# Kernel optimization log

Measured on AMD Instinct MI355X. Metric: run time of the kernel, lower is better.

Reference implementation:

```python
import jax, jax.numpy as jnp
import numpy as np

B, C, F, T, D = 8, 128, 256, 128, 32


def setup_inputs() -> dict:
    key = jax.random.key(0)
    ks = jax.random.split(key, 7)
    x = jax.random.normal(ks[0], (B, C, F, T), jnp.float32)
    # 1x1 Conv2d over the T axis == linear map on T; weights [out, T], bias [out]
    Wk = jax.random.normal(ks[1], (D, T), jnp.float32) * 0.05
    bk = jax.random.normal(ks[2], (D,), jnp.float32) * 0.05
    Wq = jax.random.normal(ks[3], (D, T), jnp.float32) * 0.05
    bq = jax.random.normal(ks[4], (D,), jnp.float32) * 0.05
    Wv = jax.random.normal(ks[5], (T, T), jnp.float32) * 0.05
    bv = jax.random.normal(ks[6], (T,), jnp.float32) * 0.05
    return {"x": x, "Wk": Wk, "bk": bk, "Wq": Wq, "bq": bq, "Wv": Wv, "bv": bv}


def _proj(xp, W, b):
    # xp: [B, C2, F, T]; W: [out, T] -> [B, F, out, C2]
    return jnp.einsum('bcft,dt->bfdc', xp, W) + b[None, None, :, None]


def reference(x, Wk, bk, Wq, bq, Wv, bv):
    C2 = x.shape[1] // 2
    xr, xi = x[:, :C2], x[:, C2:]
    k_r = _proj(xr, Wk, bk)  # [B,F,D,C2]
    k_i = _proj(xi, Wk, bk)
    q_r = _proj(xr, Wq, bq)
    q_i = _proj(xi, Wq, bq)
    v_r = _proj(xr, Wv, bv)  # [B,F,T,C2]
    v_i = _proj(xi, Wv, bv)
    # complex P = k^H... actually plain k^T q (no conjugate in source)
    P_r = jnp.einsum('bfdc,bfde->bfce', k_r, q_r) - jnp.einsum('bfdc,bfde->bfce', k_i, q_i)
    P_i = jnp.einsum('bfdc,bfde->bfce', k_r, q_i) + jnp.einsum('bfdc,bfde->bfce', k_i, q_r)
    # independent softmaxes over dim=2 (the first C2 axis)
    W_r = jax.nn.softmax(P_r, axis=2)
    W_i = jax.nn.softmax(P_i, axis=2)
    # output = v @ W (complex)
    o_r = jnp.einsum('bftc,bfce->bfte', v_r, W_r) - jnp.einsum('bftc,bfce->bfte', v_i, W_i)
    o_i = jnp.einsum('bftc,bfce->bfte', v_r, W_i) + jnp.einsum('bftc,bfce->bfte', v_i, W_r)
    # permute [B,F,T,C2] -> [B,C2,F,T], concat real/imag on channel axis
    o_r = jnp.transpose(o_r, (0, 3, 1, 2))
    o_i = jnp.transpose(o_i, (0, 3, 1, 2))
    return jnp.concatenate([o_r, o_i], axis=1)  # [B,C,F,T]
```

## Files before the change

### kernel.cpp

```cpp
#include <hip/hip_runtime.h>

typedef __attribute__((ext_vector_type(8))) __bf16 bf16x8;
typedef __attribute__((ext_vector_type(8))) unsigned short ushort8;
typedef __attribute__((ext_vector_type(4))) unsigned short ushort4v;
typedef __attribute__((ext_vector_type(4))) float f32x4;

namespace {
constexpr int kB = 8, kC = 128, kF = 256, kT = 128;

__device__ __forceinline__ int addrXT(int t, int p) { return t * 128 + (p ^ ((t & 7) << 3)); }
__device__ __forceinline__ int addrU(int ri, int e, int s) { return ri * 8192 + e * 128 + (s ^ ((e & 7) << 3)); }
__device__ __forceinline__ int addrK(int m, int c, int p) { return 16384 + m * 2048 + c * 32 + (p ^ ((c & 3) << 3)); }

__device__ __forceinline__ unsigned short b16(float f) {
    __bf16 h = (__bf16)f;
    return __builtin_bit_cast(unsigned short, h);
}

__device__ __forceinline__ bf16x8 ldfrag(const unsigned short* lds, int idx) {
    return __builtin_bit_cast(bf16x8, *(const ushort8*)(lds + idx));
}

__device__ __forceinline__ bf16x8 fneg(bf16x8 a) {
    ushort8 u = __builtin_bit_cast(ushort8, a);
    u ^= (unsigned short)0x8000;
    return __builtin_bit_cast(bf16x8, u);
}

__device__ __forceinline__ bf16x8 fragWg(const float* p) {
    f32x4 a = *(const f32x4*)p;
    f32x4 c = *(const f32x4*)(p + 4);
    bf16x8 r;
    r[0] = (__bf16)a[0]; r[1] = (__bf16)a[1]; r[2] = (__bf16)a[2]; r[3] = (__bf16)a[3];
    r[4] = (__bf16)c[0]; r[5] = (__bf16)c[1]; r[6] = (__bf16)c[2]; r[7] = (__bf16)c[3];
    return r;
}
}

__global__ __launch_bounds__(256, 4)
void chanattn_mfma2(const float* __restrict__ x,
                    const float* __restrict__ Wk, const float* __restrict__ bk,
                    const float* __restrict__ Wq, const float* __restrict__ bq,
                    const float* __restrict__ Wv, const float* __restrict__ bv,
                    float* __restrict__ out)
{
    __shared__ __align__(16) unsigned short lds[20480];

    const int f = blockIdx.x, b = blockIdx.y;
    const int tid = threadIdx.x;
    const int lane = tid & 63;
    const int w = tid >> 6;
    const int lr = lane & 15;
    const int lg = lane >> 4;
    const size_t cstr = (size_t)kF * kT;
    const float* xb = x + ((size_t)b * kC * kF + f) * kT;

    bf16x8 bqr, bqi;
    {
        bf16x8 xr_f[4], xi_f[4];
        #pragma unroll
        for (int ks = 0; ks < 4; ++ks) {
            xr_f[ks] = fragWg(xb + (size_t)(16 * w + lr) * cstr + ks * 32 + 8 * lg);
            xi_f[ks] = fragWg(xb + (size_t)(64 + 16 * w + lr) * cstr + ks * 32 + 8 * lg);
        }
        f32x4 qacc[2][2], kacc[2][2];
        #pragma unroll
        for (int ri = 0; ri < 2; ++ri)
            #pragma unroll
            for (int dt = 0; dt < 2; ++dt) {
                qacc[ri][dt] = (f32x4){0.f, 0.f, 0.f, 0.f};
                kacc[ri][dt] = (f32x4){0.f, 0.f, 0.f, 0.f};
            }
        #pragma unroll
        for (int dt = 0; dt < 2; ++dt)
            #pragma unroll
            for (int ks = 0; ks < 4; ++ks) {
                bf16x8 wq = fragWg(Wq + (size_t)(16 * dt + lr) * kT + ks * 32 + 8 * lg);
                bf16x8 wk = fragWg(Wk + (size_t)(16 * dt + lr) * kT + ks * 32 + 8 * lg);
                qacc[0][dt] = __builtin_amdgcn_mfma_f32_16x16x32_bf16(wq, xr_f[ks], qacc[0][dt], 0, 0, 0);
                qacc[1][dt] = __builtin_amdgcn_mfma_f32_16x16x32_bf16(wq, xi_f[ks], qacc[1][dt], 0, 0, 0);
                kacc[0][dt] = __builtin_amdgcn_mfma_f32_16x16x32_bf16(xr_f[ks], wk, kacc[0][dt], 0, 0, 0);
                kacc[1][dt] = __builtin_amdgcn_mfma_f32_16x16x32_bf16(xi_f[ks], wk, kacc[1][dt], 0, 0, 0);
            }
        const float bk0 = bk[lr], bk1 = bk[16 + lr];
        #pragma unroll
        for (int dt = 0; dt < 2; ++dt) {
            const int pcol = 8 * ((lr >> 2) & 3) + 4 * dt + (lr & 3);
            const float bb = dt ? bk1 : bk0;
            #pragma unroll
            for (int r = 0; r < 4; ++r) {
                const int c = 16 * w + 4 * lg + r;
                lds[addrK(0, c, pcol)] = b16(kacc[0][dt][r] + bb);
                lds[addrK(1, c, pcol)] = b16(kacc[1][dt][r] + bb);
            }
        }
        #pragma unroll
        for (int j = 0; j < 8; ++j) {
            const int dt = j >> 2, r = j & 3;
            const float bb = bq[16 * dt + 4 * lg + r];
            bqr[j] = (__bf16)(qacc[0][dt][r] + bb);
            bqi[j] = (__bf16)(qacc[1][dt][r] + bb);
        }
    }

    {
        const int c0 = 4 * (tid & 31);
        const int t0 = 4 * (tid >> 5);
        const int h  = c0 >> 6;
        const int cc = c0 & 63;
        const int p0 = 64 * h + 32 * (cc >> 5) + 8 * ((cc >> 2) & 3) + 4 * ((cc >> 4) & 1);
        #pragma unroll
        for (int tp = 0; tp < 4; ++tp) {
            const int t = t0 + 32 * tp;
            f32x4 v[4];
            #pragma unroll
            for (int j = 0; j < 4; ++j)
                v[j] = *(const f32x4*)(xb + (size_t)(c0 + j) * cstr + t);
            #pragma unroll
            for (int i = 0; i < 4; ++i) {
                ushort4v pk;
                pk[0] = b16(v[0][i]); pk[1] = b16(v[1][i]);
                pk[2] = b16(v[2][i]); pk[3] = b16(v[3][i]);
                *(ushort4v*)&lds[addrXT(t + i, p0)] = pk;
            }
        }
    }
    __syncthreads();

    f32x4 pr[4], pi[4];
    float inv_r, inv_i;
    {
        const f32x4 zero = {0.f, 0.f, 0.f, 0.f};
        #pragma unroll
        for (int ct = 0; ct < 4; ++ct) {
            bf16x8 akr = ldfrag(lds, addrK(0, ct * 16 + lr, 8 * lg));
            bf16x8 aki = ldfrag(lds, addrK(1, ct * 16 + lr, 8 * lg));
            pr[ct] = __builtin_amdgcn_mfma_f32_16x16x32_bf16(akr, bqr, zero, 0, 0, 0);
            pr[ct] = __builtin_amdgcn_mfma_f32_16x16x32_bf16(fneg(aki), bqi, pr[ct], 0, 0, 0);
            pi[ct] = __builtin_amdgcn_mfma_f32_16x16x32_bf16(akr, bqi, zero, 0, 0, 0);
            pi[ct] = __builtin_amdgcn_mfma_f32_16x16x32_bf16(aki, bqr, pi[ct], 0, 0, 0);
        }
        float mr = -1e30f, mi = -1e30f;
        #pragma unroll
        for (int ct = 0; ct < 4; ++ct)
            #pragma unroll
            for (int r = 0; r < 4; ++r) { mr = fmaxf(mr, pr[ct][r]); mi = fmaxf(mi, pi[ct][r]); }
        mr = fmaxf(mr, __shfl_xor(mr, 16)); mr = fmaxf(mr, __shfl_xor(mr, 32));
        mi = fmaxf(mi, __shfl_xor(mi, 16)); mi = fmaxf(mi, __shfl_xor(mi, 32));
        float sr = 0.f, si = 0.f;
        #pragma unroll
        for (int ct = 0; ct < 4; ++ct)
            #pragma unroll
            for (int r = 0; r < 4; ++r) {
                float er = __expf(pr[ct][r] - mr); pr[ct][r] = er; sr += er;
                float ei = __expf(pi[ct][r] - mi); pi[ct][r] = ei; si += ei;
            }
        sr += __shfl_xor(sr, 16); sr += __shfl_xor(sr, 32);
        si += __shfl_xor(si, 16); si += __shfl_xor(si, 32);
        inv_r = 1.f / sr; inv_i = 1.f / si;
    }

    bf16x8 awr[2], awi[2], awin[2];
    #pragma unroll
    for (int ks = 0; ks < 2; ++ks) {
        #pragma unroll
        for (int j = 0; j < 8; ++j) {
            const int ct = 2 * ks + (j >> 2), r = j & 3;
            awr[ks][j] = (__bf16)(pr[ct][r] * inv_r);
            awi[ks][j] = (__bf16)(pi[ct][r] * inv_i);
        }
        awin[ks] = fneg(awi[ks]);
    }

    f32x4 uacc_r[8], uacc_i[8];
    #pragma unroll
    for (int nt = 0; nt < 8; ++nt) {
        f32x4 ur = {0.f, 0.f, 0.f, 0.f}, ui = {0.f, 0.f, 0.f, 0.f};
        #pragma unroll
        for (int ks = 0; ks < 2; ++ks) {
            bf16x8 bxr = ldfrag(lds, addrXT(nt * 16 + lr, ks * 32 + 8 * lg));
            bf16x8 bxi = ldfrag(lds, addrXT(nt * 16 + lr, 64 + ks * 32 + 8 * lg));
            ur = __builtin_amdgcn_mfma_f32_16x16x32_bf16(awr[ks], bxr, ur, 0, 0, 0);
            ur = __builtin_amdgcn_mfma_f32_16x16x32_bf16(awin[ks], bxi, ur, 0, 0, 0);
            ui = __builtin_amdgcn_mfma_f32_16x16x32_bf16(awi[ks], bxr, ui, 0, 0, 0);
            ui = __builtin_amdgcn_mfma_f32_16x16x32_bf16(awr[ks], bxi, ui, 0, 0, 0);
        }
        uacc_r[nt] = ur; uacc_i[nt] = ui;
    }
    __syncthreads();
    #pragma unroll
    for (int nt = 0; nt < 8; ++nt)
        #pragma unroll
        for (int r = 0; r < 4; ++r) {
            const int e = 16 * w + 4 * lg + r;
            lds[addrU(0, e, nt * 16 + lr)] = b16(uacc_r[nt][r]);
            lds[addrU(1, e, nt * 16 + lr)] = b16(uacc_i[nt][r]);
        }
    __syncthreads();

    {
        #pragma unroll
        for (int mi_ = 0; mi_ < 2; ++mi_) {
            const int mt = 2 * w + mi_;
            bf16x8 av[4];
            #pragma unroll
            for (int ks = 0; ks < 4; ++ks)
                av[ks] = fragWg(Wv + (size_t)(mt * 16 + lr) * kT + ks * 32 + 8 * lg);
            float bvv[4];
            #pragma unroll
            for (int r = 0; r < 4; ++r) bvv[r] = 2.f * bv[mt * 16 + 4 * lg + r];

            #pragma unroll
            for (int et = 0; et < 4; ++et) {
                f32x4 aor = {0.f, 0.f, 0.f, 0.f}, aoi = {0.f, 0.f, 0.f, 0.f};
                #pragma unroll
                for (int ks = 0; ks < 4; ++ks) {
                    bf16x8 bur = ldfrag(lds, addrU(0, et * 16 + lr, ks * 32 + 8 * lg));
                    bf16x8 bui = ldfrag(lds, addrU(1, et * 16 + lr, ks * 32 + 8 * lg));
                    aor = __builtin_amdgcn_mfma_f32_16x16x32_bf16(av[ks], bur, aor, 0, 0, 0);
                    aoi = __builtin_amdgcn_mfma_f32_16x16x32_bf16(av[ks], bui, aoi, 0, 0, 0);
                }
                const int e = et * 16 + lr;
                const int tp0 = mt * 16 + 4 * lg;
                f32x4 vi;
                #pragma unroll
                for (int r = 0; r < 4; ++r) vi[r] = aoi[r] + bvv[r];
                *(f32x4*)(out + (((size_t)b * kC + e) * kF + f) * kT + tp0)      = aor;
                *(f32x4*)(out + (((size_t)b * kC + 64 + e) * kF + f) * kT + tp0) = vi;
            }
        }
    }
}

extern "C" void kernel_launch(void* const* d_in, const int* in_sizes, int n_in,
                              void* d_out, int out_size, void* d_ws, size_t ws_size,
                              hipStream_t stream) {
    const float* x  = (const float*)d_in[0];
    const float* Wk = (const float*)d_in[1];
    const float* bk = (const float*)d_in[2];
    const float* Wq = (const float*)d_in[3];
    const float* bq = (const float*)d_in[4];
    const float* Wv = (const float*)d_in[5];
    const float* bv = (const float*)d_in[6];
    float* out = (float*)d_out;

    dim3 grid(kF, kB);
    dim3 block(256);
    chanattn_mfma2<<<grid, block, 0, stream>>>(x, Wk, bk, Wq, bq, Wv, bv, out);
}
```

Measured before the change: 97.59 us.

## Pre-convert weights to bf16 fragment layout and hoist global loads earlier

Adds a small prologue kernel that converts Wk, Wq and Wv to bf16 in MFMA fragment order in the workspace, so the main kernel loads contiguous 16-byte fragments instead of converting fp32 weights per block. The x tile loads used for the LDS transpose are issued at kernel start, and the Wv fragments and bias are loaded before the barrier, so their latency overlaps with compute. The cost is an extra kernel launch and more live registers, which could reduce occupancy under the 4-blocks launch bound.

```diff
diff --git a/kernel.cpp b/kernel.cpp
--- a/kernel.cpp
+++ b/kernel.cpp
@@ -17,8 +17,8 @@
     return __builtin_bit_cast(unsigned short, h);
 }
 
-__device__ __forceinline__ bf16x8 ldfrag(const unsigned short* lds, int idx) {
-    return __builtin_bit_cast(bf16x8, *(const ushort8*)(lds + idx));
+__device__ __forceinline__ bf16x8 ldfrag(const unsigned short* p, int idx) {
+    return __builtin_bit_cast(bf16x8, *(const ushort8*)(p + idx));
 }
 
 __device__ __forceinline__ bf16x8 fneg(bf16x8 a) {
@@ -37,11 +37,30 @@
 }
 }
 
+__global__ __launch_bounds__(256)
+void conv_weights(const float* __restrict__ Wk, const float* __restrict__ Wq,
+                  const float* __restrict__ Wv, unsigned short* __restrict__ ws)
+{
+    const int fid = blockIdx.x * 256 + threadIdx.x;
+    if (fid >= 3072) return;
+    const float* src;
+    int local;
+    if (fid < 512)       { src = Wk; local = fid; }
+    else if (fid < 1024) { src = Wq; local = fid - 512; }
+    else                 { src = Wv; local = fid - 1024; }
+    const int lr = local & 15, lg = (local >> 4) & 3, ks = (local >> 6) & 3, tile = local >> 8;
+    const float* p = src + (size_t)(16 * tile + lr) * kT + ks * 32 + 8 * lg;
+    ushort8 o;
+    #pragma unroll
+    for (int j = 0; j < 8; ++j) o[j] = b16(p[j]);
+    *(ushort8*)(ws + (size_t)fid * 8) = o;
+}
+
 __global__ __launch_bounds__(256, 4)
-void chanattn_mfma2(const float* __restrict__ x,
-                    const float* __restrict__ Wk, const float* __restrict__ bk,
-                    const float* __restrict__ Wq, const float* __restrict__ bq,
-                    const float* __restrict__ Wv, const float* __restrict__ bv,
+void chanattn_mfma3(const float* __restrict__ x,
+                    const float* __restrict__ bk, const float* __restrict__ bq,
+                    const float* __restrict__ bv,
+                    const unsigned short* __restrict__ wsu,
                     float* __restrict__ out)
 {
     __shared__ __align__(16) unsigned short lds[20480];
@@ -55,14 +74,17 @@
     const size_t cstr = (size_t)kF * kT;
     const float* xb = x + ((size_t)b * kC * kF + f) * kT;
 
+    const int c0 = 4 * (tid & 31);
+    const int t0 = 4 * (tid >> 5);
+    f32x4 xv[4][4];
+    #pragma unroll
+    for (int tp = 0; tp < 4; ++tp)
+        #pragma unroll
+        for (int j = 0; j < 4; ++j)
+            xv[tp][j] = *(const f32x4*)(xb + (size_t)(c0 + j) * cstr + t0 + 32 * tp);
+
     bf16x8 bqr, bqi;
     {
-        bf16x8 xr_f[4], xi_f[4];
-        #pragma unroll
-        for (int ks = 0; ks < 4; ++ks) {
-            xr_f[ks] = fragWg(xb + (size_t)(16 * w + lr) * cstr + ks * 32 + 8 * lg);
-            xi_f[ks] = fragWg(xb + (size_t)(64 + 16 * w + lr) * cstr + ks * 32 + 8 * lg);
-        }
         f32x4 qacc[2][2], kacc[2][2];
         #pragma unroll
         for (int ri = 0; ri < 2; ++ri)
@@ -72,16 +94,19 @@
                 kacc[ri][dt] = (f32x4){0.f, 0.f, 0.f, 0.f};
             }
         #pragma unroll
-        for (int dt = 0; dt < 2; ++dt)
-            #pragma unroll
-            for (int ks = 0; ks < 4; ++ks) {
-                bf16x8 wq = fragWg(Wq + (size_t)(16 * dt + lr) * kT + ks * 32 + 8 * lg);
-                bf16x8 wk = fragWg(Wk + (size_t)(16 * dt + lr) * kT + ks * 32 + 8 * lg);
-                qacc[0][dt] = __builtin_amdgcn_mfma_f32_16x16x32_bf16(wq, xr_f[ks], qacc[0][dt], 0, 0, 0);
-                qacc[1][dt] = __builtin_amdgcn_mfma_f32_16x16x32_bf16(wq, xi_f[ks], qacc[1][dt], 0, 0, 0);
-                kacc[0][dt] = __builtin_amdgcn_mfma_f32_16x16x32_bf16(xr_f[ks], wk, kacc[0][dt], 0, 0, 0);
-                kacc[1][dt] = __builtin_amdgcn_mfma_f32_16x16x32_bf16(xi_f[ks], wk, kacc[1][dt], 0, 0, 0);
-            }
+        for (int ks = 0; ks < 4; ++ks) {
+            bf16x8 xr_f = fragWg(xb + (size_t)(16 * w + lr) * cstr + ks * 32 + 8 * lg);
+            bf16x8 xi_f = fragWg(xb + (size_t)(64 + 16 * w + lr) * cstr + ks * 32 + 8 * lg);
+            #pragma unroll
+            for (int dt = 0; dt < 2; ++dt) {
+                bf16x8 wk = ldfrag(wsu, (((dt * 4 + ks) * 4 + lg) * 16 + lr) * 8);
+                bf16x8 wq = ldfrag(wsu, 4096 + (((dt * 4 + ks) * 4 + lg) * 16 + lr) * 8);
+                qacc[0][dt] = __builtin_amdgcn_mfma_f32_16x16x32_bf16(wq, xr_f, qacc[0][dt], 0, 0, 0);
+                qacc[1][dt] = __builtin_amdgcn_mfma_f32_16x16x32_bf16(wq, xi_f, qacc[1][dt], 0, 0, 0);
+                kacc[0][dt] = __builtin_amdgcn_mfma_f32_16x16x32_bf16(xr_f, wk, kacc[0][dt], 0, 0, 0);
+                kacc[1][dt] = __builtin_amdgcn_mfma_f32_16x16x32_bf16(xi_f, wk, kacc[1][dt], 0, 0, 0);
+            }
+        }
         const float bk0 = bk[lr], bk1 = bk[16 + lr];
         #pragma unroll
         for (int dt = 0; dt < 2; ++dt) {
@@ -104,23 +129,17 @@
     }
 
     {
-        const int c0 = 4 * (tid & 31);
-        const int t0 = 4 * (tid >> 5);
         const int h  = c0 >> 6;
         const int cc = c0 & 63;
         const int p0 = 64 * h + 32 * (cc >> 5) + 8 * ((cc >> 2) & 3) + 4 * ((cc >> 4) & 1);
         #pragma unroll
         for (int tp = 0; tp < 4; ++tp) {
             const int t = t0 + 32 * tp;
-            f32x4 v[4];
-            #pragma unroll
-            for (int j = 0; j < 4; ++j)
-                v[j] = *(const f32x4*)(xb + (size_t)(c0 + j) * cstr + t);
             #pragma unroll
             for (int i = 0; i < 4; ++i) {
                 ushort4v pk;
-                pk[0] = b16(v[0][i]); pk[1] = b16(v[1][i]);
-                pk[2] = b16(v[2][i]); pk[3] = b16(v[3][i]);
+                pk[0] = b16(xv[tp][0][i]); pk[1] = b16(xv[tp][1][i]);
+                pk[2] = b16(xv[tp][2][i]); pk[3] = b16(xv[tp][3][i]);
                 *(ushort4v*)&lds[addrXT(t + i, p0)] = pk;
             }
         }
@@ -187,6 +206,19 @@
         }
         uacc_r[nt] = ur; uacc_i[nt] = ui;
     }
+
+    bf16x8 av[2][4];
+    float bvv[2][4];
+    #pragma unroll
+    for (int mi_ = 0; mi_ < 2; ++mi_) {
+        const int mt = 2 * w + mi_;
+        #pragma unroll
+        for (int ks = 0; ks < 4; ++ks)
+            av[mi_][ks] = ldfrag(wsu, 8192 + (((mt * 4 + ks) * 4 + lg) * 16 + lr) * 8);
+        #pragma unroll
+        for (int r = 0; r < 4; ++r) bvv[mi_][r] = 2.f * bv[mt * 16 + 4 * lg + r];
+    }
+
     __syncthreads();
     #pragma unroll
     for (int nt = 0; nt < 8; ++nt)
@@ -202,14 +234,6 @@
         #pragma unroll
         for (int mi_ = 0; mi_ < 2; ++mi_) {
             const int mt = 2 * w + mi_;
-            bf16x8 av[4];
-            #pragma unroll
-            for (int ks = 0; ks < 4; ++ks)
-                av[ks] = fragWg(Wv + (size_t)(mt * 16 + lr) * kT + ks * 32 + 8 * lg);
-            float bvv[4];
-            #pragma unroll
-            for (int r = 0; r < 4; ++r) bvv[r] = 2.f * bv[mt * 16 + 4 * lg + r];
-
             #pragma unroll
             for (int et = 0; et < 4; ++et) {
                 f32x4 aor = {0.f, 0.f, 0.f, 0.f}, aoi = {0.f, 0.f, 0.f, 0.f};
@@ -217,14 +241,14 @@
                 for (int ks = 0; ks < 4; ++ks) {
                     bf16x8 bur = ldfrag(lds, addrU(0, et * 16 + lr, ks * 32 + 8 * lg));
                     bf16x8 bui = ldfrag(lds, addrU(1, et * 16 + lr, ks * 32 + 8 * lg));
-                    aor = __builtin_amdgcn_mfma_f32_16x16x32_bf16(av[ks], bur, aor, 0, 0, 0);
-                    aoi = __builtin_amdgcn_mfma_f32_16x16x32_bf16(av[ks], bui, aoi, 0, 0, 0);
+                    aor = __builtin_amdgcn_mfma_f32_16x16x32_bf16(av[mi_][ks], bur, aor, 0, 0, 0);
+                    aoi = __builtin_amdgcn_mfma_f32_16x16x32_bf16(av[mi_][ks], bui, aoi, 0, 0, 0);
                 }
                 const int e = et * 16 + lr;
                 const int tp0 = mt * 16 + 4 * lg;
                 f32x4 vi;
                 #pragma unroll
-                for (int r = 0; r < 4; ++r) vi[r] = aoi[r] + bvv[r];
+                for (int r = 0; r < 4; ++r) vi[r] = aoi[r] + bvv[mi_][r];
                 *(f32x4*)(out + (((size_t)b * kC + e) * kF + f) * kT + tp0)      = aor;
                 *(f32x4*)(out + (((size_t)b * kC + 64 + e) * kF + f) * kT + tp0) = vi;
             }
@@ -243,8 +267,11 @@
     const float* Wv = (const float*)d_in[5];
     const float* bv = (const float*)d_in[6];
     float* out = (float*)d_out;
+    unsigned short* wsu = (unsigned short*)d_ws;
+
+    conv_weights<<<dim3(12), dim3(256), 0, stream>>>(Wk, Wq, Wv, wsu);
 
     dim3 grid(kF, kB);
     dim3 block(256);
-    chanattn_mfma2<<<grid, block, 0, stream>>>(x, Wk, bk, Wq, bq, Wv, bv, out);
-}
+    chanattn_mfma3<<<grid, block, 0, stream>>>(x, bk, bq, bv, wsu, out);
+}
```

After: 158.6 us. +62.5%, slower.

## Make V-projection stage wave-local and hoist x tile loads earlier

Applied to the files above, without the earlier changes.

The x tile staging loads are moved before the Q/K projection and all sixteen vector loads are issued up front, so more global loads are in flight. The U@W product now swaps the MFMA operands so each wave holds a transposed U tile. Each wave writes that tile into its own private LDS region, which removes the block-wide barrier before the final Wv projection; only a local lgkmcnt wait remains. Each wave then loops over all 8 T-tiles with its own 16 output channels. The trade-off is more Wv global loads per wave and more registers held for the early x loads.

```diff
diff --git a/kernel.cpp b/kernel.cpp
--- a/kernel.cpp
+++ b/kernel.cpp
@@ -9,16 +9,18 @@
 constexpr int kB = 8, kC = 128, kF = 256, kT = 128;
 
 __device__ __forceinline__ int addrXT(int t, int p) { return t * 128 + (p ^ ((t & 7) << 3)); }
-__device__ __forceinline__ int addrU(int ri, int e, int s) { return ri * 8192 + e * 128 + (s ^ ((e & 7) << 3)); }
 __device__ __forceinline__ int addrK(int m, int c, int p) { return 16384 + m * 2048 + c * 32 + (p ^ ((c & 3) << 3)); }
+__device__ __forceinline__ int addrUw(int w, int ri, int ep, int s) {
+    return w * 4096 + ri * 2048 + ep * 128 + (s ^ ((ep & 7) << 3));
+}
 
 __device__ __forceinline__ unsigned short b16(float f) {
     __bf16 h = (__bf16)f;
     return __builtin_bit_cast(unsigned short, h);
 }
 
-__device__ __forceinline__ bf16x8 ldfrag(const unsigned short* lds, int idx) {
-    return __builtin_bit_cast(bf16x8, *(const ushort8*)(lds + idx));
+__device__ __forceinline__ bf16x8 ldfrag(const unsigned short* p, int idx) {
+    return __builtin_bit_cast(bf16x8, *(const ushort8*)(p + idx));
 }
 
 __device__ __forceinline__ bf16x8 fneg(bf16x8 a) {
@@ -38,7 +40,7 @@
 }
 
 __global__ __launch_bounds__(256, 4)
-void chanattn_mfma2(const float* __restrict__ x,
+void chanattn_mfma4(const float* __restrict__ x,
                     const float* __restrict__ Wk, const float* __restrict__ bk,
                     const float* __restrict__ Wq, const float* __restrict__ bq,
                     const float* __restrict__ Wv, const float* __restrict__ bv,
@@ -55,6 +57,31 @@
     const size_t cstr = (size_t)kF * kT;
     const float* xb = x + ((size_t)b * kC * kF + f) * kT;
 
+    {
+        const int c0 = 4 * (tid & 31);
+        const int t0 = 4 * (tid >> 5);
+        const int h  = c0 >> 6;
+        const int cc = c0 & 63;
+        const int p0 = 64 * h + 32 * (cc >> 5) + 8 * ((cc >> 2) & 3) + 4 * ((cc >> 4) & 1);
+        f32x4 xv[4][4];
+        #pragma unroll
+        for (int tp = 0; tp < 4; ++tp)
+            #pragma unroll
+            for (int j = 0; j < 4; ++j)
+                xv[tp][j] = *(const f32x4*)(xb + (size_t)(c0 + j) * cstr + t0 + 32 * tp);
+        #pragma unroll
+        for (int tp = 0; tp < 4; ++tp) {
+            const int t = t0 + 32 * tp;
+            #pragma unroll
+            for (int i = 0; i < 4; ++i) {
+                ushort4v pk;
+                pk[0] = b16(xv[tp][0][i]); pk[1] = b16(xv[tp][1][i]);
+                pk[2] = b16(xv[tp][2][i]); pk[3] = b16(xv[tp][3][i]);
+                *(ushort4v*)&lds[addrXT(t + i, p0)] = pk;
+            }
+        }
+    }
+
     bf16x8 bqr, bqi;
     {
         bf16x8 xr_f[4], xi_f[4];
@@ -102,29 +129,6 @@
             bqi[j] = (__bf16)(qacc[1][dt][r] + bb);
         }
     }
-
-    {
-        const int c0 = 4 * (tid & 31);
-        const int t0 = 4 * (tid >> 5);
-        const int h  = c0 >> 6;
-        const int cc = c0 & 63;
-        const int p0 = 64 * h + 32 * (cc >> 5) + 8 * ((cc >> 2) & 3) + 4 * ((cc >> 4) & 1);
-        #pragma unroll
-        for (int tp = 0; tp < 4; ++tp) {
-            const int t = t0 + 32 * tp;
-            f32x4 v[4];
-            #pragma unroll
-            for (int j = 0; j < 4; ++j)
-                v[j] = *(const f32x4*)(xb + (size_t)(c0 + j) * cstr + t);
-            #pragma unroll
-            for (int i = 0; i < 4; ++i) {
-                ushort4v pk;
-                pk[0] = b16(v[0][i]); pk[1] = b16(v[1][i]);
-                pk[2] = b16(v[2][i]); pk[3] = b16(v[3][i]);
-                *(ushort4v*)&lds[addrXT(t + i, p0)] = pk;
-            }
-        }
-    }
     __syncthreads();
 
     f32x4 pr[4], pi[4];
@@ -180,55 +184,47 @@
         for (int ks = 0; ks < 2; ++ks) {
             bf16x8 bxr = ldfrag(lds, addrXT(nt * 16 + lr, ks * 32 + 8 * lg));
             bf16x8 bxi = ldfrag(lds, addrXT(nt * 16 + lr, 64 + ks * 32 + 8 * lg));
-            ur = __builtin_amdgcn_mfma_f32_16x16x32_bf16(awr[ks], bxr, ur, 0, 0, 0);
-            ur = __builtin_amdgcn_mfma_f32_16x16x32_bf16(awin[ks], bxi, ur, 0, 0, 0);
-            ui = __builtin_amdgcn_mfma_f32_16x16x32_bf16(awi[ks], bxr, ui, 0, 0, 0);
-            ui = __builtin_amdgcn_mfma_f32_16x16x32_bf16(awr[ks], bxi, ui, 0, 0, 0);
+            ur = __builtin_amdgcn_mfma_f32_16x16x32_bf16(bxr, awr[ks], ur, 0, 0, 0);
+            ur = __builtin_amdgcn_mfma_f32_16x16x32_bf16(bxi, awin[ks], ur, 0, 0, 0);
+            ui = __builtin_amdgcn_mfma_f32_16x16x32_bf16(bxr, awi[ks], ui, 0, 0, 0);
+            ui = __builtin_amdgcn_mfma_f32_16x16x32_bf16(bxi, awr[ks], ui, 0, 0, 0);
         }
         uacc_r[nt] = ur; uacc_i[nt] = ui;
     }
     __syncthreads();
-    #pragma unroll
-    for (int nt = 0; nt < 8; ++nt)
-        #pragma unroll
-        for (int r = 0; r < 4; ++r) {
-            const int e = 16 * w + 4 * lg + r;
-            lds[addrU(0, e, nt * 16 + lr)] = b16(uacc_r[nt][r]);
-            lds[addrU(1, e, nt * 16 + lr)] = b16(uacc_i[nt][r]);
-        }
-    __syncthreads();
-
-    {
-        #pragma unroll
-        for (int mi_ = 0; mi_ < 2; ++mi_) {
-            const int mt = 2 * w + mi_;
-            bf16x8 av[4];
-            #pragma unroll
-            for (int ks = 0; ks < 4; ++ks)
-                av[ks] = fragWg(Wv + (size_t)(mt * 16 + lr) * kT + ks * 32 + 8 * lg);
-            float bvv[4];
-            #pragma unroll
-            for (int r = 0; r < 4; ++r) bvv[r] = 2.f * bv[mt * 16 + 4 * lg + r];
-
-            #pragma unroll
-            for (int et = 0; et < 4; ++et) {
-                f32x4 aor = {0.f, 0.f, 0.f, 0.f}, aoi = {0.f, 0.f, 0.f, 0.f};
-                #pragma unroll
-                for (int ks = 0; ks < 4; ++ks) {
-                    bf16x8 bur = ldfrag(lds, addrU(0, et * 16 + lr, ks * 32 + 8 * lg));
-                    bf16x8 bui = ldfrag(lds, addrU(1, et * 16 + lr, ks * 32 + 8 * lg));
-                    aor = __builtin_amdgcn_mfma_f32_16x16x32_bf16(av[ks], bur, aor, 0, 0, 0);
-                    aoi = __builtin_amdgcn_mfma_f32_16x16x32_bf16(av[ks], bui, aoi, 0, 0, 0);
-                }
-                const int e = et * 16 + lr;
-                const int tp0 = mt * 16 + 4 * lg;
-                f32x4 vi;
-                #pragma unroll
-                for (int r = 0; r < 4; ++r) vi[r] = aoi[r] + bvv[r];
-                *(f32x4*)(out + (((size_t)b * kC + e) * kF + f) * kT + tp0)      = aor;
-                *(f32x4*)(out + (((size_t)b * kC + 64 + e) * kF + f) * kT + tp0) = vi;
-            }
-        }
+
+    #pragma unroll
+    for (int nt = 0; nt < 8; ++nt) {
+        ushort4v qr_, qi_;
+        #pragma unroll
+        for (int r = 0; r < 4; ++r) { qr_[r] = b16(uacc_r[nt][r]); qi_[r] = b16(uacc_i[nt][r]); }
+        const int s = nt * 16 + 4 * lg;
+        *(ushort4v*)&lds[addrUw(w, 0, lr, s)] = qr_;
+        *(ushort4v*)&lds[addrUw(w, 1, lr, s)] = qi_;
+    }
+    asm volatile("s_waitcnt lgkmcnt(0)" ::: "memory");
+
+    #pragma unroll
+    for (int mt = 0; mt < 8; ++mt) {
+        bf16x8 av[4];
+        #pragma unroll
+        for (int ks = 0; ks < 4; ++ks)
+            av[ks] = fragWg(Wv + (size_t)(16 * mt + lr) * kT + ks * 32 + 8 * lg);
+        f32x4 aor = {0.f, 0.f, 0.f, 0.f}, aoi = {0.f, 0.f, 0.f, 0.f};
+        #pragma unroll
+        for (int ks = 0; ks < 4; ++ks) {
+            bf16x8 bur = ldfrag(lds, addrUw(w, 0, lr, ks * 32 + 8 * lg));
+            bf16x8 bui = ldfrag(lds, addrUw(w, 1, lr, ks * 32 + 8 * lg));
+            aor = __builtin_amdgcn_mfma_f32_16x16x32_bf16(av[ks], bur, aor, 0, 0, 0);
+            aoi = __builtin_amdgcn_mfma_f32_16x16x32_bf16(av[ks], bui, aoi, 0, 0, 0);
+        }
+        const int e   = 16 * w + lr;
+        const int tp0 = mt * 16 + 4 * lg;
+        f32x4 vi;
+        #pragma unroll
+        for (int r = 0; r < 4; ++r) vi[r] = aoi[r] + 2.f * bv[tp0 + r];
+        *(f32x4*)(out + (((size_t)b * kC + e) * kF + f) * kT + tp0)      = aor;
+        *(f32x4*)(out + (((size_t)b * kC + 64 + e) * kF + f) * kT + tp0) = vi;
     }
 }
 
@@ -246,5 +242,5 @@
 
     dim3 grid(kF, kB);
     dim3 block(256);
-    chanattn_mfma2<<<grid, block, 0, stream>>>(x, Wk, bk, Wq, bq, Wv, bv, out);
-}
+    chanattn_mfma4<<<grid, block, 0, stream>>>(x, Wk, bk, Wq, bq, Wv, bv, out);
+}
```

Measured after the change: 147.0 us. 50.6% more time.

## Double block to 512 threads and split K/Q, U and output work across waves

Applied to the files above, without the earlier changes.

Increases the workgroup from 4 to 8 waves. The K and Q projections now run on separate wave groups, with Q passed through a new LDS region. The U GEMM and the Wv output GEMM are also split in half across the two wave groups, and the x transpose load loop is halved. This aims to shorten each block's serial critical path and raise in-block parallelism, at the cost of duplicated x fragment loads, extra LDS use and a possible drop in resident blocks per CU.

```diff
diff --git a/kernel.cpp b/kernel.cpp
--- a/kernel.cpp
+++ b/kernel.cpp
@@ -11,14 +11,15 @@
 __device__ __forceinline__ int addrXT(int t, int p) { return t * 128 + (p ^ ((t & 7) << 3)); }
 __device__ __forceinline__ int addrU(int ri, int e, int s) { return ri * 8192 + e * 128 + (s ^ ((e & 7) << 3)); }
 __device__ __forceinline__ int addrK(int m, int c, int p) { return 16384 + m * 2048 + c * 32 + (p ^ ((c & 3) << 3)); }
+__device__ __forceinline__ int addrQ(int m, int e, int p) { return 20480 + m * 2048 + e * 32 + (p ^ ((e & 3) << 3)); }
 
 __device__ __forceinline__ unsigned short b16(float f) {
     __bf16 h = (__bf16)f;
     return __builtin_bit_cast(unsigned short, h);
 }
 
-__device__ __forceinline__ bf16x8 ldfrag(const unsigned short* lds, int idx) {
-    return __builtin_bit_cast(bf16x8, *(const ushort8*)(lds + idx));
+__device__ __forceinline__ bf16x8 ldfrag(const unsigned short* p, int idx) {
+    return __builtin_bit_cast(bf16x8, *(const ushort8*)(p + idx));
 }
 
 __device__ __forceinline__ bf16x8 fneg(bf16x8 a) {
@@ -37,69 +38,82 @@
 }
 }
 
-__global__ __launch_bounds__(256, 4)
-void chanattn_mfma2(const float* __restrict__ x,
+__global__ __launch_bounds__(512, 4)
+void chanattn_mfma5(const float* __restrict__ x,
                     const float* __restrict__ Wk, const float* __restrict__ bk,
                     const float* __restrict__ Wq, const float* __restrict__ bq,
                     const float* __restrict__ Wv, const float* __restrict__ bv,
                     float* __restrict__ out)
 {
-    __shared__ __align__(16) unsigned short lds[20480];
+    __shared__ __align__(16) unsigned short lds[24576];
 
     const int f = blockIdx.x, b = blockIdx.y;
     const int tid = threadIdx.x;
     const int lane = tid & 63;
     const int w = tid >> 6;
+    const int wt = w & 3;
     const int lr = lane & 15;
     const int lg = lane >> 4;
     const size_t cstr = (size_t)kF * kT;
     const float* xb = x + ((size_t)b * kC * kF + f) * kT;
 
-    bf16x8 bqr, bqi;
     {
         bf16x8 xr_f[4], xi_f[4];
         #pragma unroll
         for (int ks = 0; ks < 4; ++ks) {
-            xr_f[ks] = fragWg(xb + (size_t)(16 * w + lr) * cstr + ks * 32 + 8 * lg);
-            xi_f[ks] = fragWg(xb + (size_t)(64 + 16 * w + lr) * cstr + ks * 32 + 8 * lg);
-        }
-        f32x4 qacc[2][2], kacc[2][2];
-        #pragma unroll
-        for (int ri = 0; ri < 2; ++ri)
+            xr_f[ks] = fragWg(xb + (size_t)(16 * wt + lr) * cstr + ks * 32 + 8 * lg);
+            xi_f[ks] = fragWg(xb + (size_t)(64 + 16 * wt + lr) * cstr + ks * 32 + 8 * lg);
+        }
+        if (w < 4) {
+            f32x4 kacc[2][2];
+            #pragma unroll
+            for (int ri = 0; ri < 2; ++ri)
+                #pragma unroll
+                for (int dt = 0; dt < 2; ++dt) kacc[ri][dt] = (f32x4){0.f, 0.f, 0.f, 0.f};
+            #pragma unroll
+            for (int dt = 0; dt < 2; ++dt)
+                #pragma unroll
+                for (int ks = 0; ks < 4; ++ks) {
+                    bf16x8 wk = fragWg(Wk + (size_t)(16 * dt + lr) * kT + ks * 32 + 8 * lg);
+                    kacc[0][dt] = __builtin_amdgcn_mfma_f32_16x16x32_bf16(xr_f[ks], wk, kacc[0][dt], 0, 0, 0);
+                    kacc[1][dt] = __builtin_amdgcn_mfma_f32_16x16x32_bf16(xi_f[ks], wk, kacc[1][dt], 0, 0, 0);
+                }
+            const float bk0 = bk[lr], bk1 = bk[16 + lr];
             #pragma unroll
             for (int dt = 0; dt < 2; ++dt) {
-                qacc[ri][dt] = (f32x4){0.f, 0.f, 0.f, 0.f};
-                kacc[ri][dt] = (f32x4){0.f, 0.f, 0.f, 0.f};
-            }
-        #pragma unroll
-        for (int dt = 0; dt < 2; ++dt)
-            #pragma unroll
-            for (int ks = 0; ks < 4; ++ks) {
-                bf16x8 wq = fragWg(Wq + (size_t)(16 * dt + lr) * kT + ks * 32 + 8 * lg);
-                bf16x8 wk = fragWg(Wk + (size_t)(16 * dt + lr) * kT + ks * 32 + 8 * lg);
-                qacc[0][dt] = __builtin_amdgcn_mfma_f32_16x16x32_bf16(wq, xr_f[ks], qacc[0][dt], 0, 0, 0);
-                qacc[1][dt] = __builtin_amdgcn_mfma_f32_16x16x32_bf16(wq, xi_f[ks], qacc[1][dt], 0, 0, 0);
-                kacc[0][dt] = __builtin_amdgcn_mfma_f32_16x16x32_bf16(xr_f[ks], wk, kacc[0][dt], 0, 0, 0);
-                kacc[1][dt] = __builtin_amdgcn_mfma_f32_16x16x32_bf16(xi_f[ks], wk, kacc[1][dt], 0, 0, 0);
-            }
-        const float bk0 = bk[lr], bk1 = bk[16 + lr];
-        #pragma unroll
-        for (int dt = 0; dt < 2; ++dt) {
-            const int pcol = 8 * ((lr >> 2) & 3) + 4 * dt + (lr & 3);
-            const float bb = dt ? bk1 : bk0;
-            #pragma unroll
-            for (int r = 0; r < 4; ++r) {
-                const int c = 16 * w + 4 * lg + r;
-                lds[addrK(0, c, pcol)] = b16(kacc[0][dt][r] + bb);
-                lds[addrK(1, c, pcol)] = b16(kacc[1][dt][r] + bb);
-            }
-        }
-        #pragma unroll
-        for (int j = 0; j < 8; ++j) {
-            const int dt = j >> 2, r = j & 3;
-            const float bb = bq[16 * dt + 4 * lg + r];
-            bqr[j] = (__bf16)(qacc[0][dt][r] + bb);
-            bqi[j] = (__bf16)(qacc[1][dt][r] + bb);
+                const int pcol = 8 * ((lr >> 2) & 3) + 4 * dt + (lr & 3);
+                const float bb = dt ? bk1 : bk0;
+                #pragma unroll
+                for (int r = 0; r < 4; ++r) {
+                    const int c = 16 * wt + 4 * lg + r;
+                    lds[addrK(0, c, pcol)] = b16(kacc[0][dt][r] + bb);
+                    lds[addrK(1, c, pcol)] = b16(kacc[1][dt][r] + bb);
+                }
+            }
+        } else {
+            f32x4 qacc[2][2];
+            #pragma unroll
+            for (int ri = 0; ri < 2; ++ri)
+                #pragma unroll
+                for (int dt = 0; dt < 2; ++dt) qacc[ri][dt] = (f32x4){0.f, 0.f, 0.f, 0.f};
+            #pragma unroll
+            for (int dt = 0; dt < 2; ++dt)
+                #pragma unroll
+                for (int ks = 0; ks < 4; ++ks) {
+                    bf16x8 wq = fragWg(Wq + (size_t)(16 * dt + lr) * kT + ks * 32 + 8 * lg);
+                    qacc[0][dt] = __builtin_amdgcn_mfma_f32_16x16x32_bf16(wq, xr_f[ks], qacc[0][dt], 0, 0, 0);
+                    qacc[1][dt] = __builtin_amdgcn_mfma_f32_16x16x32_bf16(wq, xi_f[ks], qacc[1][dt], 0, 0, 0);
+                }
+            const int e = 16 * wt + lr;
+            #pragma unroll
+            for (int dt = 0; dt < 2; ++dt)
+                #pragma unroll
+                for (int r = 0; r < 4; ++r) {
+                    const float bb = bq[16 * dt + 4 * lg + r];
+                    const int p = 8 * lg + 4 * dt + r;
+                    lds[addrQ(0, e, p)] = b16(qacc[0][dt][r] + bb);
+                    lds[addrQ(1, e, p)] = b16(qacc[1][dt][r] + bb);
+                }
         }
     }
 
@@ -110,8 +124,8 @@
         const int cc = c0 & 63;
         const int p0 = 64 * h + 32 * (cc >> 5) + 8 * ((cc >> 2) & 3) + 4 * ((cc >> 4) & 1);
         #pragma unroll
-        for (int tp = 0; tp < 4; ++tp) {
-            const int t = t0 + 32 * tp;
+        for (int tp = 0; tp < 2; ++tp) {
+            const int t = t0 + 64 * tp;
             f32x4 v[4];
             #pragma unroll
             for (int j = 0; j < 4; ++j)
@@ -131,6 +145,8 @@
     float inv_r, inv_i;
     {
         const f32x4 zero = {0.f, 0.f, 0.f, 0.f};
+        bf16x8 bqr = ldfrag(lds, addrQ(0, 16 * wt + lr, 8 * lg));
+        bf16x8 bqi = ldfrag(lds, addrQ(1, 16 * wt + lr, 8 * lg));
         #pragma unroll
         for (int ct = 0; ct < 4; ++ct) {
             bf16x8 akr = ldfrag(lds, addrK(0, ct * 16 + lr, 8 * lg));
@@ -172,9 +188,11 @@
         awin[ks] = fneg(awi[ks]);
     }
 
-    f32x4 uacc_r[8], uacc_i[8];
+    const int nth = (w >> 2) * 4;
+    f32x4 uacc_r[4], uacc_i[4];
     #pragma unroll
-    for (int nt = 0; nt < 8; ++nt) {
+    for (int nt2 = 0; nt2 < 4; ++nt2) {
+        const int nt = nth + nt2;
         f32x4 ur = {0.f, 0.f, 0.f, 0.f}, ui = {0.f, 0.f, 0.f, 0.f};
         #pragma unroll
         for (int ks = 0; ks < 2; ++ks) {
@@ -185,49 +203,48 @@
             ui = __builtin_amdgcn_mfma_f32_16x16x32_bf16(awi[ks], bxr, ui, 0, 0, 0);
             ui = __builtin_amdgcn_mfma_f32_16x16x32_bf16(awr[ks], bxi, ui, 0, 0, 0);
         }
-        uacc_r[nt] = ur; uacc_i[nt] = ui;
+        uacc_r[nt2] = ur; uacc_i[nt2] = ui;
     }
     __syncthreads();
     #pragma unroll
-    for (int nt = 0; nt < 8; ++nt)
+    for (int nt2 = 0; nt2 < 4; ++nt2) {
+        const int s = (nth + nt2) * 16 + lr;
         #pragma unroll
         for (int r = 0; r < 4; ++r) {
-            const int e = 16 * w + 4 * lg + r;
-            lds[addrU(0, e, nt * 16 + lr)] = b16(uacc_r[nt][r]);
-            lds[addrU(1, e, nt * 16 + lr)] = b16(uacc_i[nt][r]);
-        }
+            const int e = 16 * wt + 4 * lg + r;
+            lds[addrU(0, e, s)] = b16(uacc_r[nt2][r]);
+            lds[addrU(1, e, s)] = b16(uacc_i[nt2][r]);
+        }
+    }
     __syncthreads();
 
     {
-        #pragma unroll
-        for (int mi_ = 0; mi_ < 2; ++mi_) {
-            const int mt = 2 * w + mi_;
-            bf16x8 av[4];
-            #pragma unroll
-            for (int ks = 0; ks < 4; ++ks)
-                av[ks] = fragWg(Wv + (size_t)(mt * 16 + lr) * kT + ks * 32 + 8 * lg);
-            float bvv[4];
-            #pragma unroll
-            for (int r = 0; r < 4; ++r) bvv[r] = 2.f * bv[mt * 16 + 4 * lg + r];
-
-            #pragma unroll
-            for (int et = 0; et < 4; ++et) {
-                f32x4 aor = {0.f, 0.f, 0.f, 0.f}, aoi = {0.f, 0.f, 0.f, 0.f};
-                #pragma unroll
-                for (int ks = 0; ks < 4; ++ks) {
-                    bf16x8 bur = ldfrag(lds, addrU(0, et * 16 + lr, ks * 32 + 8 * lg));
-                    bf16x8 bui = ldfrag(lds, addrU(1, et * 16 + lr, ks * 32 + 8 * lg));
-                    aor = __builtin_amdgcn_mfma_f32_16x16x32_bf16(av[ks], bur, aor, 0, 0, 0);
-                    aoi = __builtin_amdgcn_mfma_f32_16x16x32_bf16(av[ks], bui, aoi, 0, 0, 0);
-                }
-                const int e = et * 16 + lr;
-                const int tp0 = mt * 16 + 4 * lg;
-                f32x4 vi;
-                #pragma unroll
-                for (int r = 0; r < 4; ++r) vi[r] = aoi[r] + bvv[r];
-                *(f32x4*)(out + (((size_t)b * kC + e) * kF + f) * kT + tp0)      = aor;
-                *(f32x4*)(out + (((size_t)b * kC + 64 + e) * kF + f) * kT + tp0) = vi;
-            }
+        const int mt = w;
+        bf16x8 av[4];
+        #pragma unroll
+        for (int ks = 0; ks < 4; ++ks)
+            av[ks] = fragWg(Wv + (size_t)(16 * mt + lr) * kT + ks * 32 + 8 * lg);
+        const int tp0 = mt * 16 + 4 * lg;
+        float bvv[4];
+        #pragma unroll
+        for (int r = 0; r < 4; ++r) bvv[r] = 2.f * bv[tp0 + r];
+
+        #pragma unroll
+        for (int et = 0; et < 4; ++et) {
+            f32x4 aor = {0.f, 0.f, 0.f, 0.f}, aoi = {0.f, 0.f, 0.f, 0.f};
+            #pragma unroll
+            for (int ks = 0; ks < 4; ++ks) {
+                bf16x8 bur = ldfrag(lds, addrU(0, et * 16 + lr, ks * 32 + 8 * lg));
+                bf16x8 bui = ldfrag(lds, addrU(1, et * 16 + lr, ks * 32 + 8 * lg));
+                aor = __builtin_amdgcn_mfma_f32_16x16x32_bf16(av[ks], bur, aor, 0, 0, 0);
+                aoi = __builtin_amdgcn_mfma_f32_16x16x32_bf16(av[ks], bui, aoi, 0, 0, 0);
+            }
+            const int e = et * 16 + lr;
+            f32x4 vi;
+            #pragma unroll
+            for (int r = 0; r < 4; ++r) vi[r] = aoi[r] + bvv[r];
+            *(f32x4*)(out + (((size_t)b * kC + e) * kF + f) * kT + tp0)      = aor;
+            *(f32x4*)(out + (((size_t)b * kC + 64 + e) * kF + f) * kT + tp0) = vi;
         }
     }
 }
@@ -245,6 +262,6 @@
     float* out = (float*)d_out;
 
     dim3 grid(kF, kB);
-    dim3 block(256);
-    chanattn_mfma2<<<grid, block, 0, stream>>>(x, Wk, bk, Wq, bq, Wv, bv, out);
-}
+    dim3 block(512);
+    chanattn_mfma5<<<grid, block, 0, stream>>>(x, Wk, bk, Wq, bq, Wv, bv, out);
+}
```

Measured after the change: 115.8 us. +18.6%, slower.
